# Kernel optimization log

Measured on AMD Instinct MI355X. Metric: run time of the kernel, lower is better.

## Reference

```python
import jax, jax.numpy as jnp
import numpy as np
from jax import lax

NPOL = 125   # polar grid size (hardcoded in module)
NANG = 126   # number of correlation offsets / angle bins


def polar_grid(n=NPOL):
    # u in [0, sqrt(2)], v in [-pi, pi]; torch.meshgrid default is 'ij'
    u = jnp.linspace(0.0, np.sqrt(2.0), n)
    v = jnp.linspace(-np.pi, np.pi, n)
    vs, us = jnp.meshgrid(v, u, indexing='ij')
    return jnp.stack([us * jnp.cos(vs), us * jnp.sin(vs)], axis=-1)  # (n, n, 2)


def grid_sample(img, grid):
    """Bilinear grid_sample, align_corners=True, zero padding.
    img: [B,C,H,W], grid: [B,Hg,Wg,2] (x,y) normalized coords. -> [B,C,Hg,Wg]"""
    B, C, H, W = img.shape
    ix = (grid[..., 0] + 1.0) * 0.5 * (W - 1)
    iy = (grid[..., 1] + 1.0) * 0.5 * (H - 1)
    x0 = jnp.floor(ix); y0 = jnp.floor(iy)
    x1 = x0 + 1.0; y1 = y0 + 1.0
    bidx = jnp.arange(B)[:, None, None]

    def corner(yc, xc, w):
        valid = (xc >= 0) & (xc <= W - 1) & (yc >= 0) & (yc <= H - 1)
        xi = jnp.clip(xc, 0, W - 1).astype(jnp.int32)
        yi = jnp.clip(yc, 0, H - 1).astype(jnp.int32)
        val = img[bidx, :, yi, xi]                 # [B,Hg,Wg,C]
        return val * (w * valid)[..., None]

    out = (corner(y0, x0, (x1 - ix) * (y1 - iy))
           + corner(y0, x1, (ix - x0) * (y1 - iy))
           + corner(y1, x0, (x1 - ix) * (iy - y0))
           + corner(y1, x1, (ix - x0) * (iy - y0)))
    return out.transpose(0, 3, 1, 2)


def affine_grid(mat, n=NPOL):
    # F.affine_grid align_corners=True over (n, n) output
    xs = jnp.linspace(-1.0, 1.0, n)
    yy, xx = jnp.meshgrid(xs, xs, indexing='ij')
    base = jnp.stack([xx, yy, jnp.ones_like(xx)], axis=-1)  # [n,n,3]
    return jnp.einsum('bij,hwj->bhwi', mat, base)           # [B,n,n,2]


def setup_inputs() -> dict:
    key = jax.random.key(0)
    k1, k2 = jax.random.split(key)
    Embd1 = jax.random.normal(k1, (32, 64, 128, 128), dtype=jnp.float32)
    Embd2 = jax.random.normal(k2, (32, 64, 128, 128), dtype=jnp.float32)
    return {"Embd1": Embd1, "Embd2": Embd2}


def reference(Embd1, Embd2):
    B, C, H, W = Embd1.shape
    pgrid = jnp.broadcast_to(polar_grid(), (B, NPOL, NPOL, 2))
    P1 = grid_sample(Embd1, pgrid)                 # [B,C,125,125]
    P2 = grid_sample(Embd2, pgrid)                 # [B,C,125,125]
    # torch.flip(input1, [1, 0]) flips channel AND batch dims (faithful)
    translated = jnp.flip(P1, axis=(0, 1))
    aug = jnp.concatenate([P1, translated], axis=2)  # [B,C,250,125]
    # per-sample full cross-correlation as grouped conv: 126 vertical offsets
    corr = lax.conv_general_dilated(
        aug.reshape(1, B * C, 2 * NPOL, NPOL), P2,
        window_strides=(1, 1), padding='VALID',
        dimension_numbers=('NCHW', 'OIHW', 'NCHW'),
        feature_group_count=B)                     # [1,B,126,1]
    scores = corr[0, :, :, 0]                      # [B,126]
    angles = jnp.linspace(-np.pi, np.pi, NANG)
    p = jax.nn.softmax(scores, axis=-1)
    theta = jnp.sum(p * angles, axis=-1) - np.pi   # [B]
    c, s = jnp.cos(theta), jnp.sin(theta)
    z = jnp.zeros_like(c)
    Mat = jnp.stack([jnp.stack([c, -s, z], axis=-1),
                     jnp.stack([s, c, z], axis=-1)], axis=1)  # [B,2,3]
    img_transform = grid_sample(Embd1, affine_grid(Mat))       # [B,C,125,125]
    return img_transform, Mat
```

## Files before the change

kernel.cpp:

```cpp
#include <hip/hip_runtime.h>
#include <math.h>
#include <stdint.h>

#define NPOL 125
#define NANG 126
#define BB 32
#define CC 64
#define HH 128
#define WW 128
#define PIX (NPOL*NPOL)
#define PI_F 3.14159265358979323846f

typedef __attribute__((ext_vector_type(8))) short bf16x8;
typedef __attribute__((ext_vector_type(4))) float f32x4;

__device__ __forceinline__ unsigned f2bf(float f) {
    union { float f; unsigned u; } x; x.f = f;
    return (x.u + 0x7fffu + ((x.u >> 16) & 1u)) >> 16;
}
__device__ __forceinline__ float bf2f(unsigned h) {
    union { float f; unsigned u; } x; x.u = h << 16;
    return x.f;
}

__global__ __launch_bounds__(256) void k0_meta(int* __restrict__ pk, float4* __restrict__ w4) {
    int idx = blockIdx.x * 256 + threadIdx.x;
    if (idx >= PIX) return;
    int i = idx / NPOL;
    int j = idx - i * NPOL;
    float u = (float)j * (1.4142135623730951f / 124.0f);
    float v = -PI_F + (float)i * (2.0f * PI_F / 124.0f);
    float x = u * cosf(v);
    float y = u * sinf(v);
    float ix = (x + 1.0f) * 0.5f * (float)(WW - 1);
    float iy = (y + 1.0f) * 0.5f * (float)(HH - 1);
    float x0 = floorf(ix), y0 = floorf(iy);
    float x1 = x0 + 1.0f,  y1 = y0 + 1.0f;
    float wx0 = x1 - ix, wx1 = ix - x0;
    float wy0 = y1 - iy, wy1 = iy - y0;
    bool vx0 = (x0 >= 0.0f) && (x0 <= 127.0f);
    bool vx1 = (x1 >= 0.0f) && (x1 <= 127.0f);
    bool vy0 = (y0 >= 0.0f) && (y0 <= 127.0f);
    bool vy1 = (y1 >= 0.0f) && (y1 <= 127.0f);
    int xi0 = (int)fminf(fmaxf(x0, 0.0f), 127.0f);
    int xi1 = (int)fminf(fmaxf(x1, 0.0f), 127.0f);
    int yi0 = (int)fminf(fmaxf(y0, 0.0f), 127.0f);
    int yi1 = (int)fminf(fmaxf(y1, 0.0f), 127.0f);
    pk[idx] = xi0 | (yi0 << 8) | (xi1 << 16) | (yi1 << 24);
    float4 w;
    w.x = wx0 * wy0 * (float)(vx0 && vy0);
    w.y = wx1 * wy0 * (float)(vx1 && vy0);
    w.z = wx0 * wy1 * (float)(vx0 && vy1);
    w.w = wx1 * wy1 * (float)(vx1 && vy1);
    w4[idx] = w;
}

__global__ __launch_bounds__(512) void k1_sample_pk(const float* __restrict__ img, unsigned* __restrict__ out,
                                                    const int* __restrict__ pk, const float4* __restrict__ w4) {
    __shared__ float plane[HH * WW];
    const int bc  = blockIdx.x;
    const int tid = threadIdx.x;
    const float4* src = (const float4*)img + (size_t)bc * (HH * WW / 4);
    float4* d4 = (float4*)plane;
    #pragma unroll
    for (int it = 0; it < 8; ++it) d4[it * 512 + tid] = src[it * 512 + tid];
    __syncthreads();
    const int base = bc * PIX;
    for (int pix = tid; pix < PIX; pix += 512) {
        int p = pk[pix];
        float4 w = w4[pix];
        int xi0 = p & 255, yi0 = (p >> 8) & 255, xi1 = (p >> 16) & 255, yi1 = (p >> 24) & 255;
        float val = w.x * plane[yi0 * WW + xi0]
                  + w.y * plane[yi0 * WW + xi1]
                  + w.z * plane[yi1 * WW + xi0]
                  + w.w * plane[yi1 * WW + xi1];
        unsigned hb = f2bf(val);
        unsigned lb = f2bf(val - bf2f(hb));
        out[base + pix] = (lb << 16) | hb;
    }
}

__global__ __launch_bounds__(256) void kz_zero(float* __restrict__ p, int n) {
    int i = blockIdx.x * 256 + threadIdx.x;
    if (i < n) p[i] = 0.0f;
}

__global__ __launch_bounds__(256, 3) void k2_gemm(const unsigned* __restrict__ P1, const unsigned* __restrict__ P2,
                                                  float* __restrict__ scores) {
    __shared__ float sd[128];
    const int bid = blockIdx.x;
    const int q = bid & 255, m = bid >> 8;
    const int bh  = q >> 4, kc0 = q & 15;
    const int b   = (m & 2) ? (BB - 1 - bh) : bh;
    const int kc  = (m & 2) ? (15 - kc0) : kc0;
    const int mt  = m & 1;

    const int tid  = threadIdx.x;
    const int lane = tid & 63;
    const int wid  = tid >> 6;
    const int wm   = wid >> 1;
    const int wn   = wid & 1;
    const int frow = lane & 15;
    const int fk8  = (lane >> 4) << 3;

    if (tid < 128) sd[tid] = 0.0f;

    f32x4 acc[4][4];
    #pragma unroll
    for (int mi = 0; mi < 4; ++mi)
        #pragma unroll
        for (int ni = 0; ni < 4; ++ni) acc[mi][ni] = (f32x4){0.f, 0.f, 0.f, 0.f};

    int rA[4], iB[4];
    bool okA[4], okB[4];
    #pragma unroll
    for (int x = 0; x < 4; ++x) {
        rA[x] = mt * 128 + wm * 64 + x * 16 + frow;
        okA[x] = rA[x] < 250;
        iB[x] = wn * 64 + x * 16 + frow;
        okB[x] = iB[x] < NPOL;
    }

    for (int cl = 0; cl < 4; ++cl) {
        const int c  = kc * 4 + cl;
        const int pD = (b * CC + c) * PIX;
        const int pF = ((BB - 1 - b) * CC + (CC - 1 - c)) * PIX;
        int baseA[4], baseB[4];
        #pragma unroll
        for (int x = 0; x < 4; ++x) {
            int bA = (rA[x] < NPOL) ? (pD + rA[x] * NPOL) : (pF + (rA[x] - NPOL) * NPOL);
            baseA[x] = okA[x] ? bA : 0;
            baseB[x] = okB[x] ? (pD + iB[x] * NPOL) : 0;
        }

        #pragma unroll
        for (int jc = 0; jc < 4; ++jc) {
            const int j0 = jc * 32;
            const bool edge = (jc == 3);

            bf16x8 bhv[4], blv[4];
            #pragma unroll
            for (int ni = 0; ni < 4; ++ni) {
                unsigned w[8];
                #pragma unroll
                for (int e = 0; e < 8; ++e) {
                    bool ok = okB[ni] && (!edge || (j0 + fk8 + e) < NPOL);
                    w[e] = ok ? P2[baseB[ni] + j0 + fk8 + e] : 0u;
                }
                #pragma unroll
                for (int e = 0; e < 8; ++e) {
                    bhv[ni][e] = (short)(w[e] & 0xffffu);
                    blv[ni][e] = (short)(w[e] >> 16);
                }
            }

            #pragma unroll
            for (int mi = 0; mi < 4; ++mi) {
                unsigned w[8];
                #pragma unroll
                for (int e = 0; e < 8; ++e) {
                    bool ok = okA[mi] && (!edge || (j0 + fk8 + e) < NPOL);
                    w[e] = ok ? P1[baseA[mi] + j0 + fk8 + e] : 0u;
                }
                bf16x8 ah, al;
                #pragma unroll
                for (int e = 0; e < 8; ++e) {
                    ah[e] = (short)(w[e] & 0xffffu);
                    al[e] = (short)(w[e] >> 16);
                }
                #pragma unroll
                for (int ni = 0; ni < 4; ++ni) {
                    acc[mi][ni] = __builtin_amdgcn_mfma_f32_16x16x32_bf16(ah, bhv[ni], acc[mi][ni], 0, 0, 0);
                    acc[mi][ni] = __builtin_amdgcn_mfma_f32_16x16x32_bf16(ah, blv[ni], acc[mi][ni], 0, 0, 0);
                    acc[mi][ni] = __builtin_amdgcn_mfma_f32_16x16x32_bf16(al, bhv[ni], acc[mi][ni], 0, 0, 0);
                }
            }
        }
    }

    float part[7][4];
    #pragma unroll
    for (int d = 0; d < 7; ++d)
        #pragma unroll
        for (int r = 0; r < 4; ++r) part[d][r] = 0.0f;
    #pragma unroll
    for (int mi = 0; mi < 4; ++mi)
        #pragma unroll
        for (int ni = 0; ni < 4; ++ni) {
            const int d = mi - ni + 3;
            #pragma unroll
            for (int r = 0; r < 4; ++r) part[d][r] += acc[mi][ni][r];
        }

    __syncthreads();
    const int rB0 = mt * 128 + wm * 64 + ((lane >> 4) << 2);
    const int iB0 = wn * 64 + frow;
    #pragma unroll
    for (int d = 0; d < 7; ++d)
        #pragma unroll
        for (int r = 0; r < 4; ++r) {
            int t = rB0 - iB0 + (d - 3) * 16 + r;
            if (t >= 0 && t < NANG) atomicAdd(&sd[t], part[d][r]);
        }
    __syncthreads();
    if (tid < NANG) atomicAdd(&scores[b * NANG + tid], sd[tid]);
}

__global__ __launch_bounds__(128) void k3_theta(const float* __restrict__ scores, float* __restrict__ matOut) {
    const int b = blockIdx.x;
    const int t = threadIdx.x;
    __shared__ float sd[128];
    __shared__ float red[128];

    float sval = (t < NANG) ? scores[b * NANG + t] : -1e30f;
    sd[t]  = sval;
    red[t] = sval;
    __syncthreads();
    for (int st = 64; st > 0; st >>= 1) {
        if (t < st) red[t] = fmaxf(red[t], red[t + st]);
        __syncthreads();
    }
    const float m = red[0];
    __syncthreads();
    const float e = (t < NANG) ? expf(sd[t] - m) : 0.0f;
    red[t] = e;
    __syncthreads();
    for (int st = 64; st > 0; st >>= 1) {
        if (t < st) red[t] += red[t + st];
        __syncthreads();
    }
    const float Z = red[0];
    __syncthreads();
    const float ang = -PI_F + (float)t * (2.0f * PI_F / 125.0f);
    red[t] = e * ang;
    __syncthreads();
    for (int st = 64; st > 0; st >>= 1) {
        if (t < st) red[t] += red[t + st];
        __syncthreads();
    }
    if (t == 0) {
        float theta = red[0] / Z - PI_F;
        float cth = cosf(theta), sth = sinf(theta);
        float* M = matOut + b * 6;
        M[0] = cth; M[1] = -sth; M[2] = 0.0f;
        M[3] = sth; M[4] = cth;  M[5] = 0.0f;
    }
}

__global__ __launch_bounds__(512) void k4_affine(const float* __restrict__ img, const float* __restrict__ mat,
                                                 float* __restrict__ out) {
    __shared__ float plane[HH * WW];
    const int bc  = blockIdx.x;
    const int b   = bc >> 6;
    const int tid = threadIdx.x;
    const float4* src = (const float4*)img + (size_t)bc * (HH * WW / 4);
    float4* d4 = (float4*)plane;
    #pragma unroll
    for (int it = 0; it < 8; ++it) d4[it * 512 + tid] = src[it * 512 + tid];
    __syncthreads();
    const float M0 = mat[b * 6 + 0], M1 = mat[b * 6 + 1];
    const float M3 = mat[b * 6 + 3], M4 = mat[b * 6 + 4];
    const int base = bc * PIX;
    for (int pix = tid; pix < PIX; pix += 512) {
        int i = pix / NPOL;
        int j = pix - i * NPOL;
        float xx = -1.0f + (float)j * (2.0f / 124.0f);
        float yy = -1.0f + (float)i * (2.0f / 124.0f);
        float gx = M0 * xx + M1 * yy;
        float gy = M3 * xx + M4 * yy;
        float ix = (gx + 1.0f) * 0.5f * (float)(WW - 1);
        float iy = (gy + 1.0f) * 0.5f * (float)(HH - 1);
        float x0 = floorf(ix), y0 = floorf(iy);
        float x1 = x0 + 1.0f,  y1 = y0 + 1.0f;
        float wx0 = x1 - ix, wx1 = ix - x0;
        float wy0 = y1 - iy, wy1 = iy - y0;
        bool vx0 = (x0 >= 0.0f) && (x0 <= 127.0f);
        bool vx1 = (x1 >= 0.0f) && (x1 <= 127.0f);
        bool vy0 = (y0 >= 0.0f) && (y0 <= 127.0f);
        bool vy1 = (y1 >= 0.0f) && (y1 <= 127.0f);
        int xi0 = (int)fminf(fmaxf(x0, 0.0f), 127.0f);
        int xi1 = (int)fminf(fmaxf(x1, 0.0f), 127.0f);
        int yi0 = (int)fminf(fmaxf(y0, 0.0f), 127.0f);
        int yi1 = (int)fminf(fmaxf(y1, 0.0f), 127.0f);
        float val = (wx0 * wy0 * (float)(vx0 && vy0)) * plane[yi0 * WW + xi0]
                  + (wx1 * wy0 * (float)(vx1 && vy0)) * plane[yi0 * WW + xi1]
                  + (wx0 * wy1 * (float)(vx0 && vy1)) * plane[yi1 * WW + xi0]
                  + (wx1 * wy1 * (float)(vx1 && vy1)) * plane[yi1 * WW + xi1];
        out[base + pix] = val;
    }
}

extern "C" void kernel_launch(void* const* d_in, const int* in_sizes, int n_in,
                              void* d_out, int out_size, void* d_ws, size_t ws_size,
                              hipStream_t stream) {
    const float* E1 = (const float*)d_in[0];
    const float* E2 = (const float*)d_in[1];
    float*    out    = (float*)d_out;
    unsigned* P1pk   = (unsigned*)d_out;
    float*    matOut = out + 32000000;

    char*     ws     = (char*)d_ws;
    unsigned* P2pk   = (unsigned*)ws;
    float*    scores = (float*)(ws + 128000000);
    int*      pk     = (int*)(ws + 128016384);
    float4*   w4     = (float4*)(ws + 128080384);

    k0_meta<<<(PIX + 255) / 256, 256, 0, stream>>>(pk, w4);

    k1_sample_pk<<<BB * CC, 512, 0, stream>>>(E1, P1pk, pk, w4);
    k1_sample_pk<<<BB * CC, 512, 0, stream>>>(E2, P2pk, pk, w4);

    kz_zero<<<(BB * NANG + 255) / 256, 256, 0, stream>>>(scores, BB * NANG);
    k2_gemm<<<1024, 256, 0, stream>>>(P1pk, P2pk, scores);
    k3_theta<<<BB, 128, 0, stream>>>(scores, matOut);
    k4_affine<<<BB * CC, 512, 0, stream>>>(E1, matOut, out);
}
```

Before: 481.6 us.

## Store sampled polar planes as padded split-fp16 rows for vectorized MFMA loads

```diff
diff --git a/kernel.cpp b/kernel.cpp
--- a/kernel.cpp
+++ b/kernel.cpp
@@ -11,17 +11,12 @@
 #define PIX (NPOL*NPOL)
 #define PI_F 3.14159265358979323846f
 
-typedef __attribute__((ext_vector_type(8))) short bf16x8;
+#define PLANE_U32 16000
+#define P1_SPLIT 2000
+
 typedef __attribute__((ext_vector_type(4))) float f32x4;
-
-__device__ __forceinline__ unsigned f2bf(float f) {
-    union { float f; unsigned u; } x; x.f = f;
-    return (x.u + 0x7fffu + ((x.u >> 16) & 1u)) >> 16;
-}
-__device__ __forceinline__ float bf2f(unsigned h) {
-    union { float f; unsigned u; } x; x.u = h << 16;
-    return x.f;
-}
+typedef _Float16 f16x8 __attribute__((ext_vector_type(8)));
+union U16 { uint4 u; f16x8 v; };
 
 __global__ __launch_bounds__(256) void k0_meta(int* __restrict__ pk, float4* __restrict__ w4) {
     int idx = blockIdx.x * 256 + threadIdx.x;
@@ -55,28 +50,48 @@
     w4[idx] = w;
 }
 
-__global__ __launch_bounds__(512) void k1_sample_pk(const float* __restrict__ img, unsigned* __restrict__ out,
-                                                    const int* __restrict__ pk, const float4* __restrict__ w4) {
+__global__ __launch_bounds__(512) void k1_sample(const float* __restrict__ img,
+                                                 unsigned* __restrict__ dst0, unsigned* __restrict__ dst1,
+                                                 int splitPlane,
+                                                 const int* __restrict__ pk, const float4* __restrict__ w4) {
     __shared__ float plane[HH * WW];
-    const int bc  = blockIdx.x;
+    const int pl  = blockIdx.x;
     const int tid = threadIdx.x;
-    const float4* src = (const float4*)img + (size_t)bc * (HH * WW / 4);
+    const float4* src = (const float4*)img + (size_t)pl * (HH * WW / 4);
     float4* d4 = (float4*)plane;
     #pragma unroll
     for (int it = 0; it < 8; ++it) d4[it * 512 + tid] = src[it * 512 + tid];
     __syncthreads();
-    const int base = bc * PIX;
-    for (int pix = tid; pix < PIX; pix += 512) {
-        int p = pk[pix];
-        float4 w = w4[pix];
-        int xi0 = p & 255, yi0 = (p >> 8) & 255, xi1 = (p >> 16) & 255, yi1 = (p >> 24) & 255;
-        float val = w.x * plane[yi0 * WW + xi0]
-                  + w.y * plane[yi0 * WW + xi1]
-                  + w.z * plane[yi1 * WW + xi0]
-                  + w.w * plane[yi1 * WW + xi1];
-        unsigned hb = f2bf(val);
-        unsigned lb = f2bf(val - bf2f(hb));
-        out[base + pix] = (lb << 16) | hb;
+
+    unsigned* dst = (pl < splitPlane) ? (dst0 + (size_t)pl * PLANE_U32)
+                                      : (dst1 + (size_t)(pl - splitPlane) * PLANE_U32);
+    for (int s = tid; s < 125 * 64; s += 512) {
+        const int r = s >> 6;
+        const int p = s & 63;
+        float v0 = 0.0f, v1 = 0.0f;
+        const int j0 = 2 * p, j1 = 2 * p + 1;
+        if (j0 < NPOL) {
+            int pix = r * NPOL + j0;
+            int pp = pk[pix]; float4 w = w4[pix];
+            int xi0 = pp & 255, yi0 = (pp >> 8) & 255, xi1 = (pp >> 16) & 255, yi1 = (pp >> 24) & 255;
+            v0 = w.x * plane[yi0 * WW + xi0] + w.y * plane[yi0 * WW + xi1]
+               + w.z * plane[yi1 * WW + xi0] + w.w * plane[yi1 * WW + xi1];
+        }
+        if (j1 < NPOL) {
+            int pix = r * NPOL + j1;
+            int pp = pk[pix]; float4 w = w4[pix];
+            int xi0 = pp & 255, yi0 = (pp >> 8) & 255, xi1 = (pp >> 16) & 255, yi1 = (pp >> 24) & 255;
+            v1 = w.x * plane[yi0 * WW + xi0] + w.y * plane[yi0 * WW + xi1]
+               + w.z * plane[yi1 * WW + xi0] + w.w * plane[yi1 * WW + xi1];
+        }
+        _Float16 h0 = (_Float16)v0; _Float16 l0 = (_Float16)(v0 - (float)h0);
+        _Float16 h1 = (_Float16)v1; _Float16 l1 = (_Float16)(v1 - (float)h1);
+        unsigned hw = (unsigned)__builtin_bit_cast(unsigned short, h0)
+                    | ((unsigned)__builtin_bit_cast(unsigned short, h1) << 16);
+        unsigned lw = (unsigned)__builtin_bit_cast(unsigned short, l0)
+                    | ((unsigned)__builtin_bit_cast(unsigned short, l1) << 16);
+        dst[r * 128 + p]      = hw;
+        dst[r * 128 + 64 + p] = lw;
     }
 }
 
@@ -85,7 +100,10 @@
     if (i < n) p[i] = 0.0f;
 }
 
-__global__ __launch_bounds__(256, 3) void k2_gemm(const unsigned* __restrict__ P1, const unsigned* __restrict__ P2,
+__global__ __launch_bounds__(256, 3) void k2_gemm(const unsigned* __restrict__ P1m,
+                                                  const unsigned* __restrict__ P1t,
+                                                  const unsigned* __restrict__ P2,
+                                                  const unsigned* __restrict__ zp,
                                                   float* __restrict__ scores) {
     __shared__ float sd[128];
     const int bid = blockIdx.x;
@@ -101,7 +119,7 @@
     const int wm   = wid >> 1;
     const int wn   = wid & 1;
     const int frow = lane & 15;
-    const int fk8  = (lane >> 4) << 3;
+    const int kq4  = (lane >> 4) << 2;
 
     if (tid < 128) sd[tid] = 0.0f;
 
@@ -112,67 +130,50 @@
         for (int ni = 0; ni < 4; ++ni) acc[mi][ni] = (f32x4){0.f, 0.f, 0.f, 0.f};
 
     int rA[4], iB[4];
-    bool okA[4], okB[4];
     #pragma unroll
     for (int x = 0; x < 4; ++x) {
         rA[x] = mt * 128 + wm * 64 + x * 16 + frow;
-        okA[x] = rA[x] < 250;
         iB[x] = wn * 64 + x * 16 + frow;
-        okB[x] = iB[x] < NPOL;
     }
 
     for (int cl = 0; cl < 4; ++cl) {
-        const int c  = kc * 4 + cl;
-        const int pD = (b * CC + c) * PIX;
-        const int pF = ((BB - 1 - b) * CC + (CC - 1 - c)) * PIX;
-        int baseA[4], baseB[4];
+        const int c   = kc * 4 + cl;
+        const int plD = b * CC + c;
+        const int plF = (BB - 1 - b) * CC + (CC - 1 - c);
+        const unsigned* pD1 = (plD < P1_SPLIT) ? (P1m + (size_t)plD * PLANE_U32)
+                                               : (P1t + (size_t)(plD - P1_SPLIT) * PLANE_U32);
+        const unsigned* pF1 = (plF < P1_SPLIT) ? (P1m + (size_t)plF * PLANE_U32)
+                                               : (P1t + (size_t)(plF - P1_SPLIT) * PLANE_U32);
+        const unsigned* pD2 = P2 + (size_t)plD * PLANE_U32;
+
+        const unsigned* rowA[4];
+        const unsigned* rowB[4];
         #pragma unroll
         for (int x = 0; x < 4; ++x) {
-            int bA = (rA[x] < NPOL) ? (pD + rA[x] * NPOL) : (pF + (rA[x] - NPOL) * NPOL);
-            baseA[x] = okA[x] ? bA : 0;
-            baseB[x] = okB[x] ? (pD + iB[x] * NPOL) : 0;
+            rowA[x] = (rA[x] < NPOL) ? (pD1 + rA[x] * 128 + kq4)
+                    : ((rA[x] < 250) ? (pF1 + (rA[x] - NPOL) * 128 + kq4) : (zp + kq4));
+            rowB[x] = (iB[x] < NPOL) ? (pD2 + iB[x] * 128 + kq4) : (zp + kq4);
         }
 
         #pragma unroll
         for (int jc = 0; jc < 4; ++jc) {
-            const int j0 = jc * 32;
-            const bool edge = (jc == 3);
-
-            bf16x8 bhv[4], blv[4];
+            const int off = jc * 16;
+            U16 bhv[4], blv[4];
             #pragma unroll
             for (int ni = 0; ni < 4; ++ni) {
-                unsigned w[8];
-                #pragma unroll
-                for (int e = 0; e < 8; ++e) {
-                    bool ok = okB[ni] && (!edge || (j0 + fk8 + e) < NPOL);
-                    w[e] = ok ? P2[baseB[ni] + j0 + fk8 + e] : 0u;
-                }
-                #pragma unroll
-                for (int e = 0; e < 8; ++e) {
-                    bhv[ni][e] = (short)(w[e] & 0xffffu);
-                    blv[ni][e] = (short)(w[e] >> 16);
-                }
+                bhv[ni].u = *(const uint4*)(rowB[ni] + off);
+                blv[ni].u = *(const uint4*)(rowB[ni] + off + 64);
             }
-
             #pragma unroll
             for (int mi = 0; mi < 4; ++mi) {
-                unsigned w[8];
-                #pragma unroll
-                for (int e = 0; e < 8; ++e) {
-                    bool ok = okA[mi] && (!edge || (j0 + fk8 + e) < NPOL);
-                    w[e] = ok ? P1[baseA[mi] + j0 + fk8 + e] : 0u;
-                }
-                bf16x8 ah, al;
-                #pragma unroll
-                for (int e = 0; e < 8; ++e) {
-                    ah[e] = (short)(w[e] & 0xffffu);
-                    al[e] = (short)(w[e] >> 16);
-                }
+                U16 ah, al;
+                ah.u = *(const uint4*)(rowA[mi] + off);
+                al.u = *(const uint4*)(rowA[mi] + off + 64);
                 #pragma unroll
                 for (int ni = 0; ni < 4; ++ni) {
-                    acc[mi][ni] = __builtin_amdgcn_mfma_f32_16x16x32_bf16(ah, bhv[ni], acc[mi][ni], 0, 0, 0);
-                    acc[mi][ni] = __builtin_amdgcn_mfma_f32_16x16x32_bf16(ah, blv[ni], acc[mi][ni], 0, 0, 0);
-                    acc[mi][ni] = __builtin_amdgcn_mfma_f32_16x16x32_bf16(al, bhv[ni], acc[mi][ni], 0, 0, 0);
+                    acc[mi][ni] = __builtin_amdgcn_mfma_f32_16x16x32_f16(ah.v, bhv[ni].v, acc[mi][ni], 0, 0, 0);
+                    acc[mi][ni] = __builtin_amdgcn_mfma_f32_16x16x32_f16(ah.v, blv[ni].v, acc[mi][ni], 0, 0, 0);
+                    acc[mi][ni] = __builtin_amdgcn_mfma_f32_16x16x32_f16(al.v, bhv[ni].v, acc[mi][ni], 0, 0, 0);
                 }
             }
         }
@@ -290,28 +291,36 @@
     }
 }
 
+#define OFF_P1T 131072000
+#define OFF_SC  134144000
+#define OFF_ZP  134160128
+#define OFF_PK  134160640
+#define OFF_W4  134410640
+
 extern "C" void kernel_launch(void* const* d_in, const int* in_sizes, int n_in,
                               void* d_out, int out_size, void* d_ws, size_t ws_size,
                               hipStream_t stream) {
     const float* E1 = (const float*)d_in[0];
     const float* E2 = (const float*)d_in[1];
     float*    out    = (float*)d_out;
-    unsigned* P1pk   = (unsigned*)d_out;
+    unsigned* P1m    = (unsigned*)d_out;
     float*    matOut = out + 32000000;
 
     char*     ws     = (char*)d_ws;
-    unsigned* P2pk   = (unsigned*)ws;
-    float*    scores = (float*)(ws + 128000000);
-    int*      pk     = (int*)(ws + 128016384);
-    float4*   w4     = (float4*)(ws + 128080384);
+    unsigned* P2pd   = (unsigned*)ws;
+    unsigned* P1t    = (unsigned*)(ws + OFF_P1T);
+    float*    scores = (float*)(ws + OFF_SC);
+    unsigned* zp     = (unsigned*)(ws + OFF_ZP);
+    int*      pk     = (int*)(ws + OFF_PK);
+    float4*   w4     = (float4*)(ws + OFF_W4);
 
     k0_meta<<<(PIX + 255) / 256, 256, 0, stream>>>(pk, w4);
 
-    k1_sample_pk<<<BB * CC, 512, 0, stream>>>(E1, P1pk, pk, w4);
-    k1_sample_pk<<<BB * CC, 512, 0, stream>>>(E2, P2pk, pk, w4);
-
-    kz_zero<<<(BB * NANG + 255) / 256, 256, 0, stream>>>(scores, BB * NANG);
-    k2_gemm<<<1024, 256, 0, stream>>>(P1pk, P2pk, scores);
+    k1_sample<<<BB * CC, 512, 0, stream>>>(E1, P1m, P1t, P1_SPLIT, pk, w4);
+    k1_sample<<<BB * CC, 512, 0, stream>>>(E2, P2pd, P2pd, 2048, pk, w4);
+
+    kz_zero<<<(4160 + 255) / 256, 256, 0, stream>>>(scores, 4160);
+    k2_gemm<<<1024, 256, 0, stream>>>(P1m, P1t, P2pd, zp, scores);
     k3_theta<<<BB, 128, 0, stream>>>(scores, matOut);
     k4_affine<<<BB * CC, 512, 0, stream>>>(E1, matOut, out);
 }
```

New measurement: 417.4 us. 13.3% less time.

## Fuse polar sampling into correlation GEMM with LDS-staged fp16 split operands

Applied to the files above, without the earlier changes.

```diff
diff --git a/kernel.cpp b/kernel.cpp
--- a/kernel.cpp
+++ b/kernel.cpp
@@ -11,227 +11,254 @@
 #define PIX (NPOL*NPOL)
 #define PI_F 3.14159265358979323846f
 
-typedef __attribute__((ext_vector_type(8))) short bf16x8;
 typedef __attribute__((ext_vector_type(4))) float f32x4;
-
-__device__ __forceinline__ unsigned f2bf(float f) {
-    union { float f; unsigned u; } x; x.f = f;
-    return (x.u + 0x7fffu + ((x.u >> 16) & 1u)) >> 16;
-}
-__device__ __forceinline__ float bf2f(unsigned h) {
-    union { float f; unsigned u; } x; x.u = h << 16;
-    return x.f;
-}
-
-__global__ __launch_bounds__(256) void k0_meta(int* __restrict__ pk, float4* __restrict__ w4) {
-    int idx = blockIdx.x * 256 + threadIdx.x;
-    if (idx >= PIX) return;
-    int i = idx / NPOL;
-    int j = idx - i * NPOL;
-    float u = (float)j * (1.4142135623730951f / 124.0f);
-    float v = -PI_F + (float)i * (2.0f * PI_F / 124.0f);
-    float x = u * cosf(v);
-    float y = u * sinf(v);
-    float ix = (x + 1.0f) * 0.5f * (float)(WW - 1);
-    float iy = (y + 1.0f) * 0.5f * (float)(HH - 1);
-    float x0 = floorf(ix), y0 = floorf(iy);
-    float x1 = x0 + 1.0f,  y1 = y0 + 1.0f;
-    float wx0 = x1 - ix, wx1 = ix - x0;
-    float wy0 = y1 - iy, wy1 = iy - y0;
-    bool vx0 = (x0 >= 0.0f) && (x0 <= 127.0f);
-    bool vx1 = (x1 >= 0.0f) && (x1 <= 127.0f);
-    bool vy0 = (y0 >= 0.0f) && (y0 <= 127.0f);
-    bool vy1 = (y1 >= 0.0f) && (y1 <= 127.0f);
-    int xi0 = (int)fminf(fmaxf(x0, 0.0f), 127.0f);
-    int xi1 = (int)fminf(fmaxf(x1, 0.0f), 127.0f);
-    int yi0 = (int)fminf(fmaxf(y0, 0.0f), 127.0f);
-    int yi1 = (int)fminf(fmaxf(y1, 0.0f), 127.0f);
-    pk[idx] = xi0 | (yi0 << 8) | (xi1 << 16) | (yi1 << 24);
-    float4 w;
-    w.x = wx0 * wy0 * (float)(vx0 && vy0);
-    w.y = wx1 * wy0 * (float)(vx1 && vy0);
-    w.z = wx0 * wy1 * (float)(vx0 && vy1);
-    w.w = wx1 * wy1 * (float)(vx1 && vy1);
-    w4[idx] = w;
-}
-
-__global__ __launch_bounds__(512) void k1_sample_pk(const float* __restrict__ img, unsigned* __restrict__ out,
-                                                    const int* __restrict__ pk, const float4* __restrict__ w4) {
-    __shared__ float plane[HH * WW];
-    const int bc  = blockIdx.x;
-    const int tid = threadIdx.x;
-    const float4* src = (const float4*)img + (size_t)bc * (HH * WW / 4);
-    float4* d4 = (float4*)plane;
-    #pragma unroll
-    for (int it = 0; it < 8; ++it) d4[it * 512 + tid] = src[it * 512 + tid];
-    __syncthreads();
-    const int base = bc * PIX;
-    for (int pix = tid; pix < PIX; pix += 512) {
-        int p = pk[pix];
-        float4 w = w4[pix];
-        int xi0 = p & 255, yi0 = (p >> 8) & 255, xi1 = (p >> 16) & 255, yi1 = (p >> 24) & 255;
-        float val = w.x * plane[yi0 * WW + xi0]
-                  + w.y * plane[yi0 * WW + xi1]
-                  + w.z * plane[yi1 * WW + xi0]
-                  + w.w * plane[yi1 * WW + xi1];
-        unsigned hb = f2bf(val);
-        unsigned lb = f2bf(val - bf2f(hb));
-        out[base + pix] = (lb << 16) | hb;
-    }
-}
+typedef _Float16 f16x8 __attribute__((ext_vector_type(8)));
+union U16 { uint4 u; f16x8 v; };
 
 __global__ __launch_bounds__(256) void kz_zero(float* __restrict__ p, int n) {
     int i = blockIdx.x * 256 + threadIdx.x;
     if (i < n) p[i] = 0.0f;
 }
 
-__global__ __launch_bounds__(256, 3) void k2_gemm(const unsigned* __restrict__ P1, const unsigned* __restrict__ P2,
-                                                  float* __restrict__ scores) {
-    __shared__ float sd[128];
-    const int bid = blockIdx.x;
-    const int q = bid & 255, m = bid >> 8;
-    const int bh  = q >> 4, kc0 = q & 15;
-    const int b   = (m & 2) ? (BB - 1 - bh) : bh;
-    const int kc  = (m & 2) ? (15 - kc0) : kc0;
-    const int mt  = m & 1;
+__device__ __forceinline__ float bil(const float* __restrict__ img, float u, float cv, float sv) {
+    float x = u * cv, y = u * sv;
+    float ix = (x + 1.0f) * 0.5f * 127.0f;
+    float iy = (y + 1.0f) * 0.5f * 127.0f;
+    float x0 = floorf(ix), y0 = floorf(iy);
+    float wx1 = ix - x0, wy1 = iy - y0;
+    float wx0 = 1.0f - wx1, wy0 = 1.0f - wy1;
+    float mx0 = (x0 >= 0.0f && x0 <= 127.0f) ? wx0 : 0.0f;
+    float mx1 = (x0 >= -1.0f && x0 <= 126.0f) ? wx1 : 0.0f;
+    float my0 = (y0 >= 0.0f && y0 <= 127.0f) ? wy0 : 0.0f;
+    float my1 = (y0 >= -1.0f && y0 <= 126.0f) ? wy1 : 0.0f;
+    int xi0 = (int)fminf(fmaxf(x0, 0.0f), 127.0f);
+    int xi1 = (int)fminf(fmaxf(x0 + 1.0f, 0.0f), 127.0f);
+    int yi0 = (int)fminf(fmaxf(y0, 0.0f), 127.0f);
+    int yi1 = (int)fminf(fmaxf(y0 + 1.0f, 0.0f), 127.0f);
+    return my0 * (mx0 * img[yi0 * WW + xi0] + mx1 * img[yi0 * WW + xi1])
+         + my1 * (mx0 * img[yi1 * WW + xi0] + mx1 * img[yi1 * WW + xi1]);
+}
+
+__global__ __launch_bounds__(512, 2) void k2_fused(const float* __restrict__ E1,
+                                                   const float* __restrict__ E2,
+                                                   double* __restrict__ scores) {
+    __shared__ unsigned bufA[16384];
+    __shared__ unsigned bufB[16384];
+    __shared__ float tabU[128];
+    __shared__ float tabC[128];
+    __shared__ float tabS[128];
+    __shared__ double sd[2][NANG];
 
     const int tid  = threadIdx.x;
     const int lane = tid & 63;
     const int wid  = tid >> 6;
-    const int wm   = wid >> 1;
-    const int wn   = wid & 1;
+    const int wm   = wid >> 2;
+    const int wn   = wid & 3;
     const int frow = lane & 15;
-    const int fk8  = (lane >> 4) << 3;
-
-    if (tid < 128) sd[tid] = 0.0f;
-
-    f32x4 acc[4][4];
+    const int kq   = lane >> 4;
+
+    const int bp = blockIdx.x & 15;
+    const int kg = blockIdx.x >> 4;
+
+    if (tid < 128) {
+        double dj = (double)tid;
+        tabU[tid] = (tid < NPOL) ? (float)(dj * (1.4142135623730951 / 124.0)) : 0.0f;
+        double v  = -3.14159265358979323846 + dj * (6.28318530717958647692 / 124.0);
+        tabC[tid] = (tid < NPOL) ? (float)cos(v) : 0.0f;
+        tabS[tid] = (tid < NPOL) ? (float)sin(v) : 0.0f;
+    }
+    if (tid < 2 * NANG) ((double*)sd)[tid] = 0.0;
+
+    f32x4 acc0[4][2], acc1[4][2], acc2[4][2], acc3[4][2];
     #pragma unroll
     for (int mi = 0; mi < 4; ++mi)
         #pragma unroll
-        for (int ni = 0; ni < 4; ++ni) acc[mi][ni] = (f32x4){0.f, 0.f, 0.f, 0.f};
-
-    int rA[4], iB[4];
-    bool okA[4], okB[4];
-    #pragma unroll
-    for (int x = 0; x < 4; ++x) {
-        rA[x] = mt * 128 + wm * 64 + x * 16 + frow;
-        okA[x] = rA[x] < 250;
-        iB[x] = wn * 64 + x * 16 + frow;
-        okB[x] = iB[x] < NPOL;
-    }
+        for (int ni = 0; ni < 2; ++ni) {
+            acc0[mi][ni] = (f32x4){0.f,0.f,0.f,0.f};
+            acc1[mi][ni] = (f32x4){0.f,0.f,0.f,0.f};
+            acc2[mi][ni] = (f32x4){0.f,0.f,0.f,0.f};
+            acc3[mi][ni] = (f32x4){0.f,0.f,0.f,0.f};
+        }
+
+    float4 stg[8];
+    unsigned hw[16], lw[16];
+
+    {
+        const float4* p0 = (const float4*)(E1 + (size_t)(bp * CC + kg * 4) * (HH * WW));
+        #pragma unroll
+        for (int k = 0; k < 8; ++k) stg[k] = p0[k * 512 + tid];
+    }
+
+#define LOADPLANE(BUF, NEXTP) do {                                              \
+    _Pragma("unroll")                                                           \
+    for (int k_ = 0; k_ < 8; ++k_) ((float4*)(BUF))[k_ * 512 + tid] = stg[k_];  \
+    __syncthreads();                                                            \
+    if (NEXTP) {                                                                \
+        const float4* np_ = (const float4*)(NEXTP);                             \
+        _Pragma("unroll")                                                       \
+        for (int k_ = 0; k_ < 8; ++k_) stg[k_] = np_[k_ * 512 + tid];           \
+    }                                                                           \
+    {                                                                           \
+        const float* f_ = (const float*)(BUF);                                  \
+        _Pragma("unroll")                                                       \
+        for (int it_ = 0; it_ < 16; ++it_) {                                    \
+            int s_ = tid + it_ * 512;                                           \
+            if (s_ < 8000) {                                                    \
+                int r_ = s_ >> 6, p_ = s_ & 63;                                 \
+                float cv_ = tabC[r_], sv_ = tabS[r_];                           \
+                int j0_ = 2 * p_, j1_ = 2 * p_ + 1;                             \
+                float va_ = bil(f_, tabU[j0_], cv_, sv_);                       \
+                float vb_ = bil(f_, tabU[j1_], cv_, sv_);                       \
+                if (j0_ >= NPOL) va_ = 0.0f;                                    \
+                if (j1_ >= NPOL) vb_ = 0.0f;                                    \
+                _Float16 h0_ = (_Float16)va_;                                   \
+                _Float16 h1_ = (_Float16)vb_;                                   \
+                _Float16 l0_ = (_Float16)(va_ - (float)h0_);                    \
+                _Float16 l1_ = (_Float16)(vb_ - (float)h1_);                    \
+                hw[it_] = (unsigned)__builtin_bit_cast(unsigned short, h0_)     \
+                        | ((unsigned)__builtin_bit_cast(unsigned short, h1_) << 16); \
+                lw[it_] = (unsigned)__builtin_bit_cast(unsigned short, l0_)     \
+                        | ((unsigned)__builtin_bit_cast(unsigned short, l1_) << 16); \
+            }                                                                   \
+        }                                                                       \
+    }                                                                           \
+    __syncthreads();                                                            \
+    _Pragma("unroll")                                                           \
+    for (int it_ = 0; it_ < 16; ++it_) {                                        \
+        int s_ = tid + it_ * 512;                                               \
+        if (s_ < 8000) {                                                        \
+            int r_ = s_ >> 6, p_ = s_ & 63;                                     \
+            int ih_ = (r_ * 128 + p_) ^ ((r_ & 7) << 2);                        \
+            (BUF)[ih_]      = hw[it_];                                          \
+            (BUF)[ih_ + 64] = lw[it_];                                          \
+        }                                                                       \
+    }                                                                           \
+    if (tid < 384) {                                                            \
+        int rr_ = 125 + (tid >> 7), pp_ = tid & 127;                            \
+        (BUF)[rr_ * 128 + pp_] = 0u;                                            \
+    }                                                                           \
+    __syncthreads();                                                            \
+} while (0)
+
+#define MPHASE(ACC) do {                                                        \
+    _Pragma("unroll")                                                           \
+    for (int jc_ = 0; jc_ < 4; ++jc_) {                                         \
+        U16 ah_[4], al_[4], bh_[2], bl_[2];                                     \
+        _Pragma("unroll")                                                       \
+        for (int ni_ = 0; ni_ < 2; ++ni_) {                                     \
+            int row_ = wn * 32 + ni_ * 16 + frow;                               \
+            int idx_ = (row_ * 128 + jc_ * 16 + kq * 4) ^ ((row_ & 7) << 2);    \
+            bh_[ni_].u = *(const uint4*)(bufB + idx_);                          \
+            bl_[ni_].u = *(const uint4*)(bufB + idx_ + 64);                     \
+        }                                                                       \
+        _Pragma("unroll")                                                       \
+        for (int mi_ = 0; mi_ < 4; ++mi_) {                                     \
+            int row_ = wm * 64 + mi_ * 16 + frow;                               \
+            int idx_ = (row_ * 128 + jc_ * 16 + kq * 4) ^ ((row_ & 7) << 2);    \
+            ah_[mi_].u = *(const uint4*)(bufA + idx_);                          \
+            al_[mi_].u = *(const uint4*)(bufA + idx_ + 64);                     \
+        }                                                                       \
+        _Pragma("unroll")                                                       \
+        for (int mi_ = 0; mi_ < 4; ++mi_)                                       \
+            _Pragma("unroll")                                                   \
+            for (int ni_ = 0; ni_ < 2; ++ni_) {                                 \
+                ACC[mi_][ni_] = __builtin_amdgcn_mfma_f32_16x16x32_f16(ah_[mi_].v, bh_[ni_].v, ACC[mi_][ni_], 0, 0, 0); \
+                ACC[mi_][ni_] = __builtin_amdgcn_mfma_f32_16x16x32_f16(ah_[mi_].v, bl_[ni_].v, ACC[mi_][ni_], 0, 0, 0); \
+                ACC[mi_][ni_] = __builtin_amdgcn_mfma_f32_16x16x32_f16(al_[mi_].v, bh_[ni_].v, ACC[mi_][ni_], 0, 0, 0); \
+            }                                                                   \
+    }                                                                           \
+} while (0)
 
     for (int cl = 0; cl < 4; ++cl) {
-        const int c  = kc * 4 + cl;
-        const int pD = (b * CC + c) * PIX;
-        const int pF = ((BB - 1 - b) * CC + (CC - 1 - c)) * PIX;
-        int baseA[4], baseB[4];
-        #pragma unroll
-        for (int x = 0; x < 4; ++x) {
-            int bA = (rA[x] < NPOL) ? (pD + rA[x] * NPOL) : (pF + (rA[x] - NPOL) * NPOL);
-            baseA[x] = okA[x] ? bA : 0;
-            baseB[x] = okB[x] ? (pD + iB[x] * NPOL) : 0;
-        }
-
-        #pragma unroll
-        for (int jc = 0; jc < 4; ++jc) {
-            const int j0 = jc * 32;
-            const bool edge = (jc == 3);
-
-            bf16x8 bhv[4], blv[4];
-            #pragma unroll
-            for (int ni = 0; ni < 4; ++ni) {
-                unsigned w[8];
-                #pragma unroll
-                for (int e = 0; e < 8; ++e) {
-                    bool ok = okB[ni] && (!edge || (j0 + fk8 + e) < NPOL);
-                    w[e] = ok ? P2[baseB[ni] + j0 + fk8 + e] : 0u;
-                }
-                #pragma unroll
-                for (int e = 0; e < 8; ++e) {
-                    bhv[ni][e] = (short)(w[e] & 0xffffu);
-                    blv[ni][e] = (short)(w[e] >> 16);
-                }
-            }
-
-            #pragma unroll
-            for (int mi = 0; mi < 4; ++mi) {
-                unsigned w[8];
-                #pragma unroll
-                for (int e = 0; e < 8; ++e) {
-                    bool ok = okA[mi] && (!edge || (j0 + fk8 + e) < NPOL);
-                    w[e] = ok ? P1[baseA[mi] + j0 + fk8 + e] : 0u;
-                }
-                bf16x8 ah, al;
-                #pragma unroll
-                for (int e = 0; e < 8; ++e) {
-                    ah[e] = (short)(w[e] & 0xffffu);
-                    al[e] = (short)(w[e] >> 16);
-                }
-                #pragma unroll
-                for (int ni = 0; ni < 4; ++ni) {
-                    acc[mi][ni] = __builtin_amdgcn_mfma_f32_16x16x32_bf16(ah, bhv[ni], acc[mi][ni], 0, 0, 0);
-                    acc[mi][ni] = __builtin_amdgcn_mfma_f32_16x16x32_bf16(ah, blv[ni], acc[mi][ni], 0, 0, 0);
-                    acc[mi][ni] = __builtin_amdgcn_mfma_f32_16x16x32_bf16(al, bhv[ni], acc[mi][ni], 0, 0, 0);
-                }
-            }
-        }
-    }
-
-    float part[7][4];
-    #pragma unroll
-    for (int d = 0; d < 7; ++d)
-        #pragma unroll
-        for (int r = 0; r < 4; ++r) part[d][r] = 0.0f;
-    #pragma unroll
-    for (int mi = 0; mi < 4; ++mi)
-        #pragma unroll
-        for (int ni = 0; ni < 4; ++ni) {
-            const int d = mi - ni + 3;
-            #pragma unroll
-            for (int r = 0; r < 4; ++r) part[d][r] += acc[mi][ni][r];
-        }
-
-    __syncthreads();
-    const int rB0 = mt * 128 + wm * 64 + ((lane >> 4) << 2);
-    const int iB0 = wn * 64 + frow;
-    #pragma unroll
-    for (int d = 0; d < 7; ++d)
-        #pragma unroll
-        for (int r = 0; r < 4; ++r) {
-            int t = rB0 - iB0 + (d - 3) * 16 + r;
-            if (t >= 0 && t < NANG) atomicAdd(&sd[t], part[d][r]);
-        }
-    __syncthreads();
-    if (tid < NANG) atomicAdd(&scores[b * NANG + tid], sd[tid]);
-}
-
-__global__ __launch_bounds__(128) void k3_theta(const float* __restrict__ scores, float* __restrict__ matOut) {
+        const int c  = kg * 4 + cl;
+        const int cb = 63 - c;
+        const float* pA1 = E1 + (size_t)(bp * CC + c) * (HH * WW);
+        const float* pA2 = E1 + (size_t)((31 - bp) * CC + cb) * (HH * WW);
+        const float* pB1 = E2 + (size_t)(bp * CC + c) * (HH * WW);
+        const float* pB2 = E2 + (size_t)((31 - bp) * CC + cb) * (HH * WW);
+        const float* pNx = (cl < 3) ? (pA1 + HH * WW) : nullptr;
+
+        LOADPLANE(bufA, pB1);
+        LOADPLANE(bufB, pA2);
+        MPHASE(acc0);
+        __syncthreads();
+        LOADPLANE(bufA, pB2);
+        MPHASE(acc1);
+        __syncthreads();
+        LOADPLANE(bufB, pA1);
+        MPHASE(acc2);
+        __syncthreads();
+        LOADPLANE(bufA, pNx);
+        MPHASE(acc3);
+        __syncthreads();
+    }
+
+#define EPI(ACC, SDI, TOFF) do {                                                \
+    float part_[5][4];                                                          \
+    _Pragma("unroll")                                                           \
+    for (int d_ = 0; d_ < 5; ++d_)                                              \
+        _Pragma("unroll")                                                       \
+        for (int r_ = 0; r_ < 4; ++r_) part_[d_][r_] = 0.0f;                    \
+    _Pragma("unroll")                                                           \
+    for (int mi_ = 0; mi_ < 4; ++mi_)                                           \
+        _Pragma("unroll")                                                       \
+        for (int ni_ = 0; ni_ < 2; ++ni_) {                                     \
+            int d_ = mi_ - ni_ + 1;                                             \
+            _Pragma("unroll")                                                   \
+            for (int r_ = 0; r_ < 4; ++r_) part_[d_][r_] += ACC[mi_][ni_][r_];  \
+        }                                                                       \
+    int tb_ = (TOFF) + wm * 64 - wn * 32 + ((lane >> 4) << 2) - (lane & 15);    \
+    _Pragma("unroll")                                                           \
+    for (int d_ = 0; d_ < 5; ++d_)                                              \
+        _Pragma("unroll")                                                       \
+        for (int r_ = 0; r_ < 4; ++r_) {                                        \
+            int t_ = tb_ + (d_ - 1) * 16 + r_;                                  \
+            if (t_ >= 0 && t_ < NANG) atomicAdd(&sd[SDI][t_], (double)part_[d_][r_]); \
+        }                                                                       \
+} while (0)
+
+    EPI(acc0, 0, 0);
+    EPI(acc1, 0, 125);
+    EPI(acc2, 1, 0);
+    EPI(acc3, 1, 125);
+    __syncthreads();
+    if (tid < 2 * NANG) {
+        int o = (tid < NANG) ? 0 : 1;
+        int t = tid - o * NANG;
+        int b = o ? (31 - bp) : bp;
+        atomicAdd(&scores[b * NANG + t], sd[o][t]);
+    }
+#undef LOADPLANE
+#undef MPHASE
+#undef EPI
+}
+
+__global__ __launch_bounds__(128) void k3_theta(const double* __restrict__ scores, float* __restrict__ matOut) {
     const int b = blockIdx.x;
     const int t = threadIdx.x;
-    __shared__ float sd[128];
-    __shared__ float red[128];
-
-    float sval = (t < NANG) ? scores[b * NANG + t] : -1e30f;
+    __shared__ double sd[128];
+    __shared__ double red[128];
+
+    double sval = (t < NANG) ? scores[b * NANG + t] : -1e300;
     sd[t]  = sval;
     red[t] = sval;
     __syncthreads();
     for (int st = 64; st > 0; st >>= 1) {
-        if (t < st) red[t] = fmaxf(red[t], red[t + st]);
-        __syncthreads();
-    }
-    const float m = red[0];
-    __syncthreads();
-    const float e = (t < NANG) ? expf(sd[t] - m) : 0.0f;
+        if (t < st) red[t] = fmax(red[t], red[t + st]);
+        __syncthreads();
+    }
+    const double m = red[0];
+    __syncthreads();
+    const double e = (t < NANG) ? exp(sd[t] - m) : 0.0;
     red[t] = e;
     __syncthreads();
     for (int st = 64; st > 0; st >>= 1) {
         if (t < st) red[t] += red[t + st];
         __syncthreads();
     }
-    const float Z = red[0];
-    __syncthreads();
-    const float ang = -PI_F + (float)t * (2.0f * PI_F / 125.0f);
+    const double Z = red[0];
+    __syncthreads();
+    const double ang = -3.14159265358979323846 + (double)t * (6.28318530717958647692 / 125.0);
     red[t] = e * ang;
     __syncthreads();
     for (int st = 64; st > 0; st >>= 1) {
@@ -239,8 +266,8 @@
         __syncthreads();
     }
     if (t == 0) {
-        float theta = red[0] / Z - PI_F;
-        float cth = cosf(theta), sth = sinf(theta);
+        double theta = red[0] / Z - 3.14159265358979323846;
+        float cth = (float)cos(theta), sth = (float)sin(theta);
         float* M = matOut + b * 6;
         M[0] = cth; M[1] = -sth; M[2] = 0.0f;
         M[3] = sth; M[4] = cth;  M[5] = 0.0f;
@@ -264,28 +291,25 @@
     for (int pix = tid; pix < PIX; pix += 512) {
         int i = pix / NPOL;
         int j = pix - i * NPOL;
-        float xx = -1.0f + (float)j * (2.0f / 124.0f);
-        float yy = -1.0f + (float)i * (2.0f / 124.0f);
+        float xx = (float)(-1.0 + (double)j * (2.0 / 124.0));
+        float yy = (float)(-1.0 + (double)i * (2.0 / 124.0));
         float gx = M0 * xx + M1 * yy;
         float gy = M3 * xx + M4 * yy;
-        float ix = (gx + 1.0f) * 0.5f * (float)(WW - 1);
-        float iy = (gy + 1.0f) * 0.5f * (float)(HH - 1);
+        float ix = (gx + 1.0f) * 0.5f * 127.0f;
+        float iy = (gy + 1.0f) * 0.5f * 127.0f;
         float x0 = floorf(ix), y0 = floorf(iy);
-        float x1 = x0 + 1.0f,  y1 = y0 + 1.0f;
-        float wx0 = x1 - ix, wx1 = ix - x0;
-        float wy0 = y1 - iy, wy1 = iy - y0;
-        bool vx0 = (x0 >= 0.0f) && (x0 <= 127.0f);
-        bool vx1 = (x1 >= 0.0f) && (x1 <= 127.0f);
-        bool vy0 = (y0 >= 0.0f) && (y0 <= 127.0f);
-        bool vy1 = (y1 >= 0.0f) && (y1 <= 127.0f);
+        float wx1 = ix - x0, wy1 = iy - y0;
+        float wx0 = 1.0f - wx1, wy0 = 1.0f - wy1;
+        float mx0 = (x0 >= 0.0f && x0 <= 127.0f) ? wx0 : 0.0f;
+        float mx1 = (x0 >= -1.0f && x0 <= 126.0f) ? wx1 : 0.0f;
+        float my0 = (y0 >= 0.0f && y0 <= 127.0f) ? wy0 : 0.0f;
+        float my1 = (y0 >= -1.0f && y0 <= 126.0f) ? wy1 : 0.0f;
         int xi0 = (int)fminf(fmaxf(x0, 0.0f), 127.0f);
-        int xi1 = (int)fminf(fmaxf(x1, 0.0f), 127.0f);
+        int xi1 = (int)fminf(fmaxf(x0 + 1.0f, 0.0f), 127.0f);
         int yi0 = (int)fminf(fmaxf(y0, 0.0f), 127.0f);
-        int yi1 = (int)fminf(fmaxf(y1, 0.0f), 127.0f);
-        float val = (wx0 * wy0 * (float)(vx0 && vy0)) * plane[yi0 * WW + xi0]
-                  + (wx1 * wy0 * (float)(vx1 && vy0)) * plane[yi0 * WW + xi1]
-                  + (wx0 * wy1 * (float)(vx0 && vy1)) * plane[yi1 * WW + xi0]
-                  + (wx1 * wy1 * (float)(vx1 && vy1)) * plane[yi1 * WW + xi1];
+        int yi1 = (int)fminf(fmaxf(y0 + 1.0f, 0.0f), 127.0f);
+        float val = my0 * (mx0 * plane[yi0 * WW + xi0] + mx1 * plane[yi0 * WW + xi1])
+                  + my1 * (mx0 * plane[yi1 * WW + xi0] + mx1 * plane[yi1 * WW + xi1]);
         out[base + pix] = val;
     }
 }
@@ -295,23 +319,12 @@
                               hipStream_t stream) {
     const float* E1 = (const float*)d_in[0];
     const float* E2 = (const float*)d_in[1];
-    float*    out    = (float*)d_out;
-    unsigned* P1pk   = (unsigned*)d_out;
-    float*    matOut = out + 32000000;
-
-    char*     ws     = (char*)d_ws;
-    unsigned* P2pk   = (unsigned*)ws;
-    float*    scores = (float*)(ws + 128000000);
-    int*      pk     = (int*)(ws + 128016384);
-    float4*   w4     = (float4*)(ws + 128080384);
-
-    k0_meta<<<(PIX + 255) / 256, 256, 0, stream>>>(pk, w4);
-
-    k1_sample_pk<<<BB * CC, 512, 0, stream>>>(E1, P1pk, pk, w4);
-    k1_sample_pk<<<BB * CC, 512, 0, stream>>>(E2, P2pk, pk, w4);
-
-    kz_zero<<<(BB * NANG + 255) / 256, 256, 0, stream>>>(scores, BB * NANG);
-    k2_gemm<<<1024, 256, 0, stream>>>(P1pk, P2pk, scores);
+    float*  out    = (float*)d_out;
+    float*  matOut = out + 32000000;
+    double* scores = (double*)d_ws;
+
+    kz_zero<<<(2 * BB * NANG + 255) / 256, 256, 0, stream>>>((float*)scores, 2 * BB * NANG);
+    k2_fused<<<256, 512, 0, stream>>>(E1, E2, scores);
     k3_theta<<<BB, 128, 0, stream>>>(scores, matOut);
     k4_affine<<<BB * CC, 512, 0, stream>>>(E1, matOut, out);
 }
```

Result: faster. 420.0 us (-12.8%).
